# Optimization experiments

Hardware: AMD Instinct MI355X
Metric: run time of the kernel (lower is better)

## Reference

```python
import jax, jax.numpy as jnp
import numpy as np

N, E, D, H, K = 8192, 8, 1024, 4096, 2


def setup_inputs() -> dict:
    key = jax.random.key(0)
    ks = jax.random.split(key, 12)
    s = 0.02  # init scale for weights
    return {
        "x": jax.random.normal(ks[0], (N, D), jnp.float32),
        "noise": jax.random.normal(ks[1], (N, E), jnp.float32),
        "Wg_w": jax.random.normal(ks[2], (D, E), jnp.float32) * s,
        "Wg_b": jnp.zeros((E,), jnp.float32),
        "Wn_w": jax.random.normal(ks[3], (D, E), jnp.float32) * s,
        "Wn_b": jnp.zeros((E,), jnp.float32),
        "w1": jax.random.normal(ks[4], (E, D, H), jnp.float32) * s,
        "b1": jnp.zeros((E, H), jnp.float32),
        "w2": jax.random.normal(ks[5], (E, H, D), jnp.float32) * s,
        "b2": jnp.zeros((E, D), jnp.float32),
        "k": K,
    }


def reference(x, noise, Wg_w, Wg_b, Wn_w, Wn_b, w1, b1, w2, b2, k):
    # --- noisy top-k gating: H(x) = Wg(x) + noise * softplus(Wn(x)) ---
    g_logits = x @ Wg_w + Wg_b                       # [N, E]
    n_scale = jax.nn.softplus(x @ Wn_w + Wn_b)       # [N, E]
    h = g_logits + noise * n_scale                   # [N, E]
    topk_vals, topk_inds = jax.lax.top_k(h, k)       # [N, k]
    gates = jax.nn.softmax(topk_vals, axis=-1)       # [N, k]

    # Scatter top-k gates into a dense [N, E] map (zeros for unselected experts),
    # so the weighted combine is exactly sum_j gates[n,j] * expert_{inds[n,j]}(x_n).
    n_tok, n_exp = h.shape
    dense_gates = jnp.zeros((n_tok, n_exp), h.dtype).at[
        jnp.arange(n_tok)[:, None], topk_inds
    ].set(gates)                                     # [N, E]

    # --- per-expert 2-layer MLP: fc2(relu(fc1(x))) ---
    hid = jax.nn.relu(jnp.einsum('nd,edh->neh', x, w1) + b1)  # [N, E, H]
    y = jnp.einsum('neh,ehd->ned', hid, w2) + b2              # [N, E, D]
    out = jnp.einsum('ned,ne->nd', y, dense_gates)            # [N, D]
    return out
```

## Files before the change

kernel.cpp:

```cpp
#include <hip/hip_runtime.h>
#include <hip/hip_bf16.h>

#define NTOK 8192
#define NEXP 8
#define DMODEL 1024
#define DHID 4096

typedef __bf16 bf16x8 __attribute__((ext_vector_type(8)));
typedef float f32x4 __attribute__((ext_vector_type(4)));

__device__ __forceinline__ unsigned short f2bf(float f) {
  return __builtin_bit_cast(unsigned short, __float2bfloat16(f));
}

__device__ __forceinline__ void gload_lds16(const void* g, void* l) {
  __builtin_amdgcn_global_load_lds(
      (const __attribute__((address_space(1))) unsigned int*)g,
      (__attribute__((address_space(3))) unsigned int*)l, 16, 0, 0);
}

__device__ __forceinline__ int imin(int a, int b) { return a < b ? a : b; }

constexpr size_t OFF_XB   = 0;
constexpr size_t OFF_W1T  = OFF_XB + (size_t)NTOK * DMODEL * 2;
constexpr size_t OFF_W2T  = OFF_W1T + (size_t)NEXP * DHID * DMODEL * 2;
constexpr size_t OFF_HID  = OFF_W2T + (size_t)NEXP * DMODEL * DHID * 2;
constexpr size_t OFF_IDX  = OFF_HID + (size_t)NTOK * 2 * DHID * 2;
constexpr size_t OFF_GATE = OFF_IDX + (size_t)NTOK * 2 * 4;
constexpr size_t OFF_LIST = OFF_GATE + (size_t)NTOK * 2 * 4;
constexpr size_t OFF_CNT  = OFF_LIST + (size_t)NTOK * 2 * 4;
constexpr size_t OFF_OFFS = OFF_CNT + 128;
constexpr size_t OFF_CUR  = OFF_OFFS + 128;

__global__ __launch_bounds__(256) void prep_kernel(
    const float* __restrict__ w1, const float* __restrict__ w2,
    unsigned short* __restrict__ w1t, unsigned short* __restrict__ w2t,
    const float* __restrict__ x, const float* __restrict__ noise,
    const float* __restrict__ Wg_w, const float* __restrict__ Wg_b,
    const float* __restrict__ Wn_w, const float* __restrict__ Wn_b,
    unsigned short* __restrict__ xb, int* __restrict__ topk_idx,
    float* __restrict__ topk_gate, int* __restrict__ counts) {
  __shared__ float sh[64][65];
  const int bid = blockIdx.x;

  if (bid < 16384) {
    const float* in;
    unsigned short* outp;
    int R, C, r0, c0;
    if (bid < 8192) {
      int e = bid >> 10, rem = bid & 1023;
      R = DMODEL; C = DHID;
      in = w1 + (size_t)e * R * C;
      outp = w1t + (size_t)e * R * C;
      r0 = (rem >> 6) * 64;
      c0 = (rem & 63) * 64;
    } else {
      int t = bid - 8192;
      int e = t >> 10, rem = t & 1023;
      R = DHID; C = DMODEL;
      in = w2 + (size_t)e * R * C;
      outp = w2t + (size_t)e * R * C;
      r0 = (rem >> 4) * 64;
      c0 = (rem & 15) * 64;
    }
    int tx = threadIdx.x & 15, ty = threadIdx.x >> 4;
#pragma unroll
    for (int p = 0; p < 4; ++p) {
      int row = ty + p * 16;
      float4 v = *(const float4*)&in[(size_t)(r0 + row) * C + c0 + tx * 4];
      sh[row][tx * 4 + 0] = v.x;
      sh[row][tx * 4 + 1] = v.y;
      sh[row][tx * 4 + 2] = v.z;
      sh[row][tx * 4 + 3] = v.w;
    }
    __syncthreads();
#pragma unroll
    for (int p = 0; p < 4; ++p) {
      int crow = ty + p * 16;
      ushort4 o;
      o.x = f2bf(sh[tx * 4 + 0][crow]);
      o.y = f2bf(sh[tx * 4 + 1][crow]);
      o.z = f2bf(sh[tx * 4 + 2][crow]);
      o.w = f2bf(sh[tx * 4 + 3][crow]);
      *(ushort4*)&outp[(size_t)(c0 + crow) * R + r0 + tx * 4] = o;
    }
    return;
  }

  int g = bid - 16384;
  int wave = threadIdx.x >> 6;
  int lane = threadIdx.x & 63;
  int n = g * 4 + wave;
  if (n >= NTOK) return;

  float ag[8] = {0.f, 0.f, 0.f, 0.f, 0.f, 0.f, 0.f, 0.f};
  float an[8] = {0.f, 0.f, 0.f, 0.f, 0.f, 0.f, 0.f, 0.f};
  const float* xr = x + (size_t)n * DMODEL;
  unsigned short* xbr = xb + (size_t)n * DMODEL;
#pragma unroll 4
  for (int i = 0; i < DMODEL / 64; ++i) {
    int d = lane + i * 64;
    float xv = xr[d];
    xbr[d] = f2bf(xv);
    const float4* wg = (const float4*)(Wg_w + (size_t)d * 8);
    const float4* wn = (const float4*)(Wn_w + (size_t)d * 8);
    float4 g0 = wg[0], g1 = wg[1];
    float4 n0 = wn[0], n1 = wn[1];
    ag[0] += xv * g0.x; ag[1] += xv * g0.y; ag[2] += xv * g0.z; ag[3] += xv * g0.w;
    ag[4] += xv * g1.x; ag[5] += xv * g1.y; ag[6] += xv * g1.z; ag[7] += xv * g1.w;
    an[0] += xv * n0.x; an[1] += xv * n0.y; an[2] += xv * n0.z; an[3] += xv * n0.w;
    an[4] += xv * n1.x; an[5] += xv * n1.y; an[6] += xv * n1.z; an[7] += xv * n1.w;
  }
#pragma unroll
  for (int off = 32; off > 0; off >>= 1) {
#pragma unroll
    for (int j = 0; j < 8; ++j) {
      ag[j] += __shfl_down(ag[j], off, 64);
      an[j] += __shfl_down(an[j], off, 64);
    }
  }
  if (lane == 0) {
    float h[8];
#pragma unroll
    for (int e = 0; e < 8; ++e) {
      float gl = ag[e] + Wg_b[e];
      float z = an[e] + Wn_b[e];
      float sp = fmaxf(z, 0.f) + log1pf(expf(-fabsf(z)));
      h[e] = gl + noise[(size_t)n * 8 + e] * sp;
    }
    int i0 = 0; float v0 = h[0];
#pragma unroll
    for (int e = 1; e < 8; ++e)
      if (h[e] > v0) { v0 = h[e]; i0 = e; }
    int i1 = -1; float v1 = -1e30f;
#pragma unroll
    for (int e = 0; e < 8; ++e)
      if (e != i0 && h[e] > v1) { v1 = h[e]; i1 = e; }
    float e1 = expf(v1 - v0);
    float inv = 1.f / (1.f + e1);
    topk_idx[n * 2] = i0;
    topk_idx[n * 2 + 1] = i1;
    topk_gate[n * 2] = inv;
    topk_gate[n * 2 + 1] = e1 * inv;
    atomicAdd(&counts[i0], 1);
    atomicAdd(&counts[i1], 1);
  }
}

__global__ void scan_kernel(const int* __restrict__ counts,
                            int* __restrict__ offsets, int* __restrict__ cursor) {
  if (threadIdx.x == 0) {
    int acc = 0;
    for (int e = 0; e < NEXP; ++e) {
      offsets[e] = acc;
      cursor[e] = acc;
      acc += counts[e];
    }
    offsets[NEXP] = acc;
  }
}

__global__ void scatter_kernel(const int* __restrict__ topk_idx,
                               int* __restrict__ cursor, int* __restrict__ list) {
  int n = blockIdx.x * 256 + threadIdx.x;
  if (n >= NTOK) return;
#pragma unroll
  for (int j = 0; j < 2; ++j) {
    int e = topk_idx[n * 2 + j];
    int pos = atomicAdd(&cursor[e], 1);
    list[pos] = n * 2 + j;
  }
}

#define VMW(N) asm volatile("s_waitcnt vmcnt(" #N ")" ::: "memory")

template <int MODE>
__global__ __launch_bounds__(256, 4) void expert_gemm(
    const unsigned short* __restrict__ Asrc, const unsigned short* __restrict__ Bt,
    const float* __restrict__ bias, const int* __restrict__ offsets,
    const int* __restrict__ list, const float* __restrict__ gates,
    unsigned short* __restrict__ hid, float* __restrict__ out) {
  constexpr int Krow = MODE ? DHID : DMODEL;
  constexpr int Nout = MODE ? DMODEL : DHID;
  constexpr int NT = Krow / 32;

  const int gx = gridDim.x, gy = gridDim.y;
  const int lin = blockIdx.x + gx * (blockIdx.y + gy * blockIdx.z);
  const int e = lin & 7;
  int r = lin >> 3;

  int by, bx;
  if (MODE == 0) {
    int st = r >> 6;
    int inner = r & 63;
    int sm = st >> 2, sn = st & 3;
    if (sm & 1) sn = 3 - sn;
    by = sm * 8 + (inner >> 3);
    bx = sn * 8 + (inner & 7);
  } else {
    by = r & 63;
    bx = r >> 6;
  }

  const int off = offsets[e];
  const int ne = offsets[e + 1] - off;
  const int m0 = by * 128;
  if (m0 >= ne) return;
  const int n0 = bx * 128;

  __shared__ alignas(16) unsigned short Al[3][128 * 32];
  __shared__ alignas(16) unsigned short Bl[3][128 * 32];

  const int tid = threadIdx.x;
  const int lane = tid & 63;
  const int w = tid >> 6;
  const int wm = (w >> 1) * 64;
  const int wn = (w & 1) * 64;
  const int lr = lane & 15;
  const int kg = lane >> 4;
  const int chrd = (kg ^ ((lr >> 1) & 3)) * 8;

  const unsigned short* srcA[2];
  const unsigned short* srcB[2];
#pragma unroll
  for (int i = 0; i < 2; ++i) {
    int q = tid + i * 256;
    int rr = q >> 2, c = q & 3;
    int cs = c ^ ((rr >> 1) & 3);
    int p = off + imin(m0 + rr, ne - 1);
    if (MODE == 0) {
      int token = list[p] >> 1;
      srcA[i] = Asrc + (size_t)token * DMODEL + cs * 8;
    } else {
      srcA[i] = Asrc + (size_t)p * DHID + cs * 8;
    }
    srcB[i] = Bt + (size_t)e * Nout * Krow + (size_t)(n0 + rr) * Krow + cs * 8;
  }

  f32x4 acc[4][4] = {};

  auto stage = [&](int slot, int kt) {
#pragma unroll
    for (int i = 0; i < 2; ++i) {
      int q = tid + i * 256;
      gload_lds16(srcA[i] + kt * 32, &Al[slot][q * 8]);
      gload_lds16(srcB[i] + kt * 32, &Bl[slot][q * 8]);
    }
  };

  auto compute = [&](int slot) {
    bf16x8 af[4], bfr[4];
#pragma unroll
    for (int mf = 0; mf < 4; ++mf)
      af[mf] = *(const bf16x8*)&Al[slot][(wm + mf * 16 + lr) * 32 + chrd];
#pragma unroll
    for (int nf = 0; nf < 4; ++nf)
      bfr[nf] = *(const bf16x8*)&Bl[slot][(wn + nf * 16 + lr) * 32 + chrd];
    asm volatile("s_waitcnt lgkmcnt(0)" ::: "memory");
    __builtin_amdgcn_sched_barrier(0);
#pragma unroll
    for (int mf = 0; mf < 4; ++mf)
#pragma unroll
      for (int nf = 0; nf < 4; ++nf)
        acc[mf][nf] = __builtin_amdgcn_mfma_f32_16x16x32_bf16(af[mf], bfr[nf],
                                                              acc[mf][nf], 0, 0, 0);
  };

  stage(0, 0);
  stage(1, 1);
  stage(2, 2);

  int cur = 0;
  for (int t = 0; t < NT; ++t) {
    if (t < NT - 2) { VMW(8); }
    else if (t == NT - 2) { VMW(4); }
    else { VMW(0); }
    __builtin_amdgcn_s_barrier();
    __builtin_amdgcn_sched_barrier(0);
    compute(cur);
    asm volatile("s_waitcnt lgkmcnt(0)" ::: "memory");
    __builtin_amdgcn_sched_barrier(0);
    __builtin_amdgcn_s_barrier();
    if (t + 3 < NT) stage(cur, t + 3);
    cur = (cur == 2) ? 0 : cur + 1;
  }

  if (MODE == 0) {
#pragma unroll
    for (int mf = 0; mf < 4; ++mf) {
#pragma unroll
      for (int j = 0; j < 4; ++j) {
        int rloc = wm + mf * 16 + kg * 4 + j;
        int row = m0 + rloc;
        if (row < ne) {
          size_t p = (size_t)(off + row);
#pragma unroll
          for (int nf = 0; nf < 4; ++nf) {
            int col = n0 + wn + nf * 16 + lr;
            float v = acc[mf][nf][j] + bias[(size_t)e * Nout + col];
            hid[p * DHID + col] = f2bf(fmaxf(v, 0.f));
          }
        }
      }
    }
  } else {
#pragma unroll
    for (int mf = 0; mf < 4; ++mf) {
#pragma unroll
      for (int j = 0; j < 4; ++j) {
        int rloc = wm + mf * 16 + kg * 4 + j;
        int row = m0 + rloc;
        if (row < ne) {
          int lv = list[off + row];
          int token = lv >> 1;
          float g = gates[lv];
#pragma unroll
          for (int nf = 0; nf < 4; ++nf) {
            int col = n0 + wn + nf * 16 + lr;
            float v = (acc[mf][nf][j] + bias[(size_t)e * Nout + col]) * g;
            atomicAdd(&out[(size_t)token * DMODEL + col], v);
          }
        }
      }
    }
  }
}

extern "C" void kernel_launch(void* const* d_in, const int* in_sizes, int n_in,
                              void* d_out, int out_size, void* d_ws, size_t ws_size,
                              hipStream_t stream) {
  const float* x = (const float*)d_in[0];
  const float* noise = (const float*)d_in[1];
  const float* Wg_w = (const float*)d_in[2];
  const float* Wg_b = (const float*)d_in[3];
  const float* Wn_w = (const float*)d_in[4];
  const float* Wn_b = (const float*)d_in[5];
  const float* w1 = (const float*)d_in[6];
  const float* b1 = (const float*)d_in[7];
  const float* w2 = (const float*)d_in[8];
  const float* b2 = (const float*)d_in[9];
  float* out = (float*)d_out;

  char* ws = (char*)d_ws;
  unsigned short* xb = (unsigned short*)(ws + OFF_XB);
  unsigned short* w1t = (unsigned short*)(ws + OFF_W1T);
  unsigned short* w2t = (unsigned short*)(ws + OFF_W2T);
  unsigned short* hid = (unsigned short*)(ws + OFF_HID);
  int* topk_idx = (int*)(ws + OFF_IDX);
  float* topk_gate = (float*)(ws + OFF_GATE);
  int* list = (int*)(ws + OFF_LIST);
  int* counts = (int*)(ws + OFF_CNT);
  int* offsets = (int*)(ws + OFF_OFFS);
  int* cursor = (int*)(ws + OFF_CUR);

  hipMemsetAsync(out, 0, (size_t)NTOK * DMODEL * sizeof(float), stream);
  hipMemsetAsync(counts, 0, NEXP * sizeof(int), stream);

  prep_kernel<<<18432, 256, 0, stream>>>(w1, w2, w1t, w2t, x, noise, Wg_w, Wg_b,
                                         Wn_w, Wn_b, xb, topk_idx, topk_gate,
                                         counts);
  scan_kernel<<<1, 64, 0, stream>>>(counts, offsets, cursor);
  scatter_kernel<<<NTOK / 256, 256, 0, stream>>>(topk_idx, cursor, list);

  expert_gemm<0><<<dim3(32, 64, NEXP), 256, 0, stream>>>(
      xb, w1t, b1, offsets, list, topk_gate, hid, nullptr);
  expert_gemm<1><<<dim3(8, 64, NEXP), 256, 0, stream>>>(
      hid, w2t, b2, offsets, list, topk_gate, nullptr, out);
}
```

Measured before the change: 827.1 us.

## Move w2 transpose-convert into the first expert GEMM launch to overlap

The fp32-to-bf16 transpose of w2 moves out of the prep kernel and into extra blocks appended to the first expert GEMM grid, which is flattened to 1D. The goal is to let the memory-bound w2 conversion run alongside the compute-bound fc1 GEMM, and to shorten the prep kernel that sits in front of the scan and scatter steps. The transpose reuses the GEMM's LDS buffer as scratch. The risk is that the conversion blocks compete with GEMM blocks for bandwidth and CU slots.

Measured after the change: 813.2 us, median of 2. About the same (-1.7%).

```diff
diff --git a/kernel.cpp b/kernel.cpp
--- a/kernel.cpp
+++ b/kernel.cpp
@@ -33,8 +33,7 @@
 constexpr size_t OFF_CUR  = OFF_OFFS + 128;
 
 __global__ __launch_bounds__(256) void prep_kernel(
-    const float* __restrict__ w1, const float* __restrict__ w2,
-    unsigned short* __restrict__ w1t, unsigned short* __restrict__ w2t,
+    const float* __restrict__ w1, unsigned short* __restrict__ w1t,
     const float* __restrict__ x, const float* __restrict__ noise,
     const float* __restrict__ Wg_w, const float* __restrict__ Wg_b,
     const float* __restrict__ Wn_w, const float* __restrict__ Wn_b,
@@ -43,26 +42,13 @@
   __shared__ float sh[64][65];
   const int bid = blockIdx.x;
 
-  if (bid < 16384) {
-    const float* in;
-    unsigned short* outp;
-    int R, C, r0, c0;
-    if (bid < 8192) {
-      int e = bid >> 10, rem = bid & 1023;
-      R = DMODEL; C = DHID;
-      in = w1 + (size_t)e * R * C;
-      outp = w1t + (size_t)e * R * C;
-      r0 = (rem >> 6) * 64;
-      c0 = (rem & 63) * 64;
-    } else {
-      int t = bid - 8192;
-      int e = t >> 10, rem = t & 1023;
-      R = DHID; C = DMODEL;
-      in = w2 + (size_t)e * R * C;
-      outp = w2t + (size_t)e * R * C;
-      r0 = (rem >> 4) * 64;
-      c0 = (rem & 15) * 64;
-    }
+  if (bid < 8192) {
+    int e = bid >> 10, rem = bid & 1023;
+    const int R = DMODEL, C = DHID;
+    const float* in = w1 + (size_t)e * R * C;
+    unsigned short* outp = w1t + (size_t)e * R * C;
+    int r0 = (rem >> 6) * 64;
+    int c0 = (rem & 63) * 64;
     int tx = threadIdx.x & 15, ty = threadIdx.x >> 4;
 #pragma unroll
     for (int p = 0; p < 4; ++p) {
@@ -87,7 +73,7 @@
     return;
   }
 
-  int g = bid - 16384;
+  int g = bid - 8192;
   int wave = threadIdx.x >> 6;
   int lane = threadIdx.x & 63;
   int n = g * 4 + wave;
@@ -179,13 +165,51 @@
     const unsigned short* __restrict__ Asrc, const unsigned short* __restrict__ Bt,
     const float* __restrict__ bias, const int* __restrict__ offsets,
     const int* __restrict__ list, const float* __restrict__ gates,
-    unsigned short* __restrict__ hid, float* __restrict__ out) {
+    unsigned short* __restrict__ hid, float* __restrict__ out,
+    const float* __restrict__ w2src, unsigned short* __restrict__ w2dst) {
   constexpr int Krow = MODE ? DHID : DMODEL;
   constexpr int Nout = MODE ? DMODEL : DHID;
   constexpr int NT = Krow / 32;
 
+  __shared__ alignas(16) unsigned short Al[3][128 * 32];
+  __shared__ alignas(16) unsigned short Bl[3][128 * 32];
+
   const int gx = gridDim.x, gy = gridDim.y;
   const int lin = blockIdx.x + gx * (blockIdx.y + gy * blockIdx.z);
+
+  if (MODE == 0 && lin >= 16384) {
+    float (*sh)[65] = reinterpret_cast<float(*)[65]>(&Al[0][0]);
+    int t = lin - 16384;
+    int e = t >> 10, rem = t & 1023;
+    const int R = DHID, C = DMODEL;
+    const float* in = w2src + (size_t)e * R * C;
+    unsigned short* outp = w2dst + (size_t)e * R * C;
+    int r0 = (rem >> 4) * 64;
+    int c0 = (rem & 15) * 64;
+    int tx = threadIdx.x & 15, ty = threadIdx.x >> 4;
+#pragma unroll
+    for (int p = 0; p < 4; ++p) {
+      int row = ty + p * 16;
+      float4 v = *(const float4*)&in[(size_t)(r0 + row) * C + c0 + tx * 4];
+      sh[row][tx * 4 + 0] = v.x;
+      sh[row][tx * 4 + 1] = v.y;
+      sh[row][tx * 4 + 2] = v.z;
+      sh[row][tx * 4 + 3] = v.w;
+    }
+    __syncthreads();
+#pragma unroll
+    for (int p = 0; p < 4; ++p) {
+      int crow = ty + p * 16;
+      ushort4 o;
+      o.x = f2bf(sh[tx * 4 + 0][crow]);
+      o.y = f2bf(sh[tx * 4 + 1][crow]);
+      o.z = f2bf(sh[tx * 4 + 2][crow]);
+      o.w = f2bf(sh[tx * 4 + 3][crow]);
+      *(ushort4*)&outp[(size_t)(c0 + crow) * R + r0 + tx * 4] = o;
+    }
+    return;
+  }
+
   const int e = lin & 7;
   int r = lin >> 3;
 
@@ -207,9 +231,6 @@
   const int m0 = by * 128;
   if (m0 >= ne) return;
   const int n0 = bx * 128;
-
-  __shared__ alignas(16) unsigned short Al[3][128 * 32];
-  __shared__ alignas(16) unsigned short Bl[3][128 * 32];
 
   const int tid = threadIdx.x;
   const int lane = tid & 63;
@@ -356,14 +377,14 @@
   hipMemsetAsync(out, 0, (size_t)NTOK * DMODEL * sizeof(float), stream);
   hipMemsetAsync(counts, 0, NEXP * sizeof(int), stream);
 
-  prep_kernel<<<18432, 256, 0, stream>>>(w1, w2, w1t, w2t, x, noise, Wg_w, Wg_b,
+  prep_kernel<<<10240, 256, 0, stream>>>(w1, w1t, x, noise, Wg_w, Wg_b,
                                          Wn_w, Wn_b, xb, topk_idx, topk_gate,
                                          counts);
   scan_kernel<<<1, 64, 0, stream>>>(counts, offsets, cursor);
   scatter_kernel<<<NTOK / 256, 256, 0, stream>>>(topk_idx, cursor, list);
 
-  expert_gemm<0><<<dim3(32, 64, NEXP), 256, 0, stream>>>(
-      xb, w1t, b1, offsets, list, topk_gate, hid, nullptr);
+  expert_gemm<0><<<dim3(24576, 1, 1), 256, 0, stream>>>(
+      xb, w1t, b1, offsets, list, topk_gate, hid, nullptr, w2, w2t);
   expert_gemm<1><<<dim3(8, 64, NEXP), 256, 0, stream>>>(
-      hid, w2t, b2, offsets, list, topk_gate, nullptr, out);
-}
+      hid, w2t, b2, offsets, list, topk_gate, nullptr, out, nullptr, nullptr);
+}
```
